# Kernel tuning notes

Hardware: AMD Instinct MI355X
Metric: run time of the kernel (lower is better)

The kernel has to match this reference:

```python
import jax, jax.numpy as jnp
import numpy as np

N_HEADS = 16
HEAD_DIM = 64
ROPE_BASE = 10000.0


def _apply_rope(x, offset):
    # x: (B, T, H, hd); rotates consecutive pairs (x[2i], x[2i+1]) as complex numbers,
    # matching torch.view_as_complex on reshape(..., -1, 2).
    B, T, H, hd = x.shape
    inv_freq = 1.0 / (ROPE_BASE ** (jnp.arange(0, hd, 2, dtype=jnp.float32) / hd))  # (hd/2,)
    t = jnp.arange(T, dtype=jnp.float32) + offset
    ang = t[:, None] * inv_freq[None, :]                      # (T, hd/2)
    cos = jnp.cos(ang)[None, :, None, :]                      # (1, T, 1, hd/2)
    sin = jnp.sin(ang)[None, :, None, :]
    x1 = x[..., 0::2]
    x2 = x[..., 1::2]
    out = jnp.stack([x1 * cos - x2 * sin, x1 * sin + x2 * cos], axis=-1)
    return out.reshape(B, T, H, hd).astype(x.dtype)


def setup_inputs() -> dict:
    key = jax.random.key(0)
    ks = jax.random.split(key, 5)
    D = N_HEADS * HEAD_DIM  # 1024
    s = 1.0 / np.sqrt(D)
    x = jax.random.normal(ks[0], (2, 2048, D), jnp.float32)
    Wqkv = jax.random.normal(ks[1], (D, 3 * D), jnp.float32) * s
    bqkv = jax.random.normal(ks[2], (3 * D,), jnp.float32) * 0.01
    Wout = jax.random.normal(ks[3], (D, D), jnp.float32) * s
    bout = jax.random.normal(ks[4], (D,), jnp.float32) * 0.01
    return {"x": x, "Wqkv": Wqkv, "bqkv": bqkv, "Wout": Wout, "bout": bout, "offset": 0}


def reference(x, Wqkv, bqkv, Wout, bout, offset):
    B, T, D = x.shape
    qkv = (x @ Wqkv + bqkv).reshape(B, T, 3, N_HEADS, HEAD_DIM)
    q, k, v = qkv[:, :, 0], qkv[:, :, 1], qkv[:, :, 2]       # (B, T, H, hd)
    q = _apply_rope(q, offset)
    k = _apply_rope(k, offset)
    # kv_cache is None and T == window_size, so no crop occurs.
    new_cache = jnp.stack([k, v], axis=1)                     # (B, 2, T, H, hd)
    scale = 1.0 / np.sqrt(HEAD_DIM)
    scores = jnp.einsum("bqhd,bkhd->bhqk", q, k) * scale      # (B, H, T, T)
    mask = jnp.tril(jnp.ones((T, T), dtype=bool))
    scores = jnp.where(mask[None, None], scores, jnp.finfo(scores.dtype).min)
    attn = jax.nn.softmax(scores, axis=-1)
    ctx = jnp.einsum("bhqk,bkhd->bqhd", attn, v).reshape(B, T, D)
    out = ctx @ Wout + bout
    return (out, new_cache)
```

## Files before the change

### kernel.cpp

```cpp
#include <hip/hip_runtime.h>
#include <stdint.h>
#include <math.h>


typedef __bf16 bf16_t;
typedef bf16_t bf16x8 __attribute__((ext_vector_type(8)));
typedef float f32x4 __attribute__((ext_vector_type(4)));
typedef unsigned short ushort8_t __attribute__((ext_vector_type(8)));

__device__ __forceinline__ unsigned short f2bf(float f) {
    union { float f; unsigned int i; } v; v.f = f;
    unsigned int r = v.i + 0x7fffu + ((v.i >> 16) & 1u);
    return (unsigned short)(r >> 16);
}
__device__ __forceinline__ bf16x8 ld8(const unsigned short* p) {
    return *(const bf16x8*)p;
}
__device__ __forceinline__ void gload_lds16(const unsigned short* g, unsigned short* l) {
    __builtin_amdgcn_global_load_lds(
        (__attribute__((address_space(1))) void*)(g),
        (__attribute__((address_space(3))) void*)(l),
        16, 0, 0);
}

__global__ void k_cvt(const float* __restrict__ in, unsigned short* __restrict__ out) {
    const int i = (blockIdx.x * 256 + threadIdx.x) * 8;
    float4 a = *(const float4*)&in[i];
    float4 b = *(const float4*)&in[i + 4];
    ushort8_t v;
    v[0] = f2bf(a.x); v[1] = f2bf(a.y); v[2] = f2bf(a.z); v[3] = f2bf(a.w);
    v[4] = f2bf(b.x); v[5] = f2bf(b.y); v[6] = f2bf(b.z); v[7] = f2bf(b.w);
    *(ushort8_t*)&out[i] = v;
}

__global__ void k_ropetab(float* __restrict__ tab, const int* __restrict__ offp) {
    int idx = blockIdx.x * blockDim.x + threadIdx.x;
    int t = idx >> 5, i = idx & 31;
    float off = (float)(*offp);
    float inv = powf(10000.0f, -(float)(2 * i) / 64.0f);
    float ang = ((float)t + off) * inv;
    float s, c;
    sincosf(ang, &s, &c);
    tab[idx * 2]     = c;
    tab[idx * 2 + 1] = s;
}

__global__ void k_transposeF2B(const float* __restrict__ in,
                               unsigned short* __restrict__ out, int R, int C) {
    __shared__ __align__(16) float tile[64 * 68];
    const int bz = blockIdx.z;
    const size_t base = (size_t)bz * R * C;
    const int tR = blockIdx.y * 64, tC = blockIdx.x * 64;
    const int tid = threadIdx.x;
#pragma unroll
    for (int it = 0; it < 4; ++it) {
        int flat = (it * 256 + tid) * 4;
        int r = flat >> 6, c = flat & 63;
        *(float4*)&tile[r * 68 + c] =
            *(const float4*)&in[base + (size_t)(tR + r) * C + tC + c];
    }
    __syncthreads();
#pragma unroll
    for (int it = 0; it < 2; ++it) {
        int flat = (it * 256 + tid) * 8;
        int rr = flat >> 6, cc = flat & 63;
        ushort8_t v;
#pragma unroll
        for (int j = 0; j < 8; ++j) v[j] = f2bf(tile[(cc + j) * 68 + rr]);
        *(ushort8_t*)&out[base + (size_t)(tC + rr) * R + tR + cc] = v;
    }
}

__global__ void k_transpose64(const unsigned short* __restrict__ in,
                              unsigned short* __restrict__ out, int R, int C) {
    __shared__ __align__(16) unsigned short tile[64 * 72];
    const int bz = blockIdx.z;
    const size_t base = (size_t)bz * R * C;
    const int tR = blockIdx.y * 64, tC = blockIdx.x * 64;
    const int tid = threadIdx.x;
#pragma unroll
    for (int it = 0; it < 2; ++it) {
        int flat = (it * 256 + tid) * 8;
        int r = flat >> 6, c = flat & 63;
        *(ushort8_t*)&tile[r * 72 + c] =
            *(const ushort8_t*)&in[base + (size_t)(tR + r) * C + tC + c];
    }
    __syncthreads();
#pragma unroll
    for (int it = 0; it < 2; ++it) {
        int flat = (it * 256 + tid) * 8;
        int rr = flat >> 6, cc = flat & 63;
        ushort8_t v;
#pragma unroll
        for (int j = 0; j < 8; ++j) v[j] = tile[(cc + j) * 72 + rr];
        *(ushort8_t*)&out[base + (size_t)(tC + rr) * R + tR + cc] = v;
    }
}

template <int EPI>
__global__ __launch_bounds__(512, 2) void k_gemm(
    const unsigned short* __restrict__ A,
    const unsigned short* __restrict__ Bt,
    const float* __restrict__ bias,
    const float* __restrict__ tab,
    unsigned short* __restrict__ oq,
    unsigned short* __restrict__ ok,
    unsigned short* __restrict__ ov,
    float* __restrict__ cache,
    float* __restrict__ outp)
{
    constexpr int K = 1024;
    __shared__ __align__(16) unsigned short lds[65536];
    unsigned short* lA = lds;
    unsigned short* lB = lds + 32768;

    const int tid  = threadIdx.x;
    const int lane = tid & 63, w = tid >> 6;
    const int wr = w >> 2, wc = w & 3;
    const int lrow = lane & 15, quad = lane >> 4;

    const int gx  = gridDim.x;
    const int nwg = gx * gridDim.y;
    const int bid = blockIdx.y * gx + blockIdx.x;
    const int sw  = (bid & 7) * (nwg >> 3) + (bid >> 3);
    const int blockM = (sw / gx) * 256;
    const int blockN = (sw % gx) * 256;

    const int q8    = (lane & 7) ^ (lane >> 3);
    const int srow0 = ((w * 16 + (lane >> 3)) << 1) + ((q8 >> 2) & 1);
    const int scol  = (q8 & 3) * 8;
    const unsigned short* srcA = A  + (size_t)(blockM + srow0) * K + scol;
    const unsigned short* srcB = Bt + (size_t)(blockN + srow0) * K + scol;
    unsigned short* dA = lA + w * 1024;
    unsigned short* dB = lB + w * 1024;

    const int rp   = lrow >> 1;
    const int swzu = ((((lane & 1) << 6) | (quad << 4)) ^ (rp << 4)) >> 1;

    f32x4 acc[8][4];
#pragma unroll
    for (int m = 0; m < 8; ++m)
#pragma unroll
        for (int n = 0; n < 4; ++n) acc[m][n] = (f32x4){0.f, 0.f, 0.f, 0.f};

#define STAGE_A(T, KH) do { \
        const unsigned short* s_ = srcA + (T) * 64 + (KH) * 32; \
        unsigned short* d_ = dA + (((2*(T)+(KH)) & 3) << 13); \
        gload_lds16(s_, d_); \
        gload_lds16(s_ + 16 * K, d_ + 512); } while (0)
#define STAGE_B(T, KH) do { \
        const unsigned short* s_ = srcB + (T) * 64 + (KH) * 32; \
        unsigned short* d_ = dB + (((2*(T)+(KH)) & 3) << 13); \
        gload_lds16(s_, d_); \
        gload_lds16(s_ + 16 * K, d_ + 512); } while (0)
#define WAITN(n) asm volatile("s_waitcnt vmcnt(" #n ")" ::: "memory")
#define RD_A(slot) do { \
        _Pragma("unroll") \
        for (int m = 0; m < 8; ++m) \
            aA[m] = ld8(&lA[((slot) << 13) + (wr * 64 + m * 8 + rp) * 64 + swzu]); } while (0)
#define RD_B(slot, nh) do { \
        _Pragma("unroll") \
        for (int nl = 0; nl < 2; ++nl) \
            bB[nl] = ld8(&lB[((slot) << 13) + (wc * 32 + (nh) * 16 + nl * 8 + rp) * 64 + swzu]); } while (0)
#define MFMA16(nh) do { \
        __builtin_amdgcn_s_barrier(); \
        asm volatile("s_waitcnt lgkmcnt(0)" ::: "memory"); \
        __builtin_amdgcn_sched_barrier(0); \
        __builtin_amdgcn_s_setprio(1); \
        _Pragma("unroll") \
        for (int m = 0; m < 8; ++m) { \
            acc[m][(nh)*2+0] = __builtin_amdgcn_mfma_f32_16x16x32_bf16(aA[m], bB[0], acc[m][(nh)*2+0], 0, 0, 0); \
            acc[m][(nh)*2+1] = __builtin_amdgcn_mfma_f32_16x16x32_bf16(aA[m], bB[1], acc[m][(nh)*2+1], 0, 0, 0); } \
        __builtin_amdgcn_s_setprio(0); \
        __builtin_amdgcn_s_barrier(); } while (0)

    STAGE_A(0, 0); STAGE_B(0, 0);
    STAGE_A(0, 1); STAGE_B(0, 1);
    STAGE_A(1, 0); STAGE_B(1, 0);
    STAGE_A(1, 1);
    asm volatile("s_waitcnt vmcnt(8)" ::: "memory");
    __builtin_amdgcn_s_barrier();

    bf16x8 aA[8], bB[2];
    for (int i = 0; i < 7; ++i) {
        const int E = 2 * i, O = 2 * i + 1;
        WAITN(6); RD_A(0); RD_B(0, 0); STAGE_B(O, 1);     MFMA16(0);
        RD_B(0, 1);                    STAGE_A(E + 2, 0); MFMA16(1);
        WAITN(6); RD_A(1); RD_B(1, 0); STAGE_B(E + 2, 0); MFMA16(0);
        RD_B(1, 1);                    STAGE_A(E + 2, 1); MFMA16(1);
        WAITN(6); RD_A(2); RD_B(2, 0); STAGE_B(E + 2, 1); MFMA16(0);
        RD_B(2, 1);                    STAGE_A(O + 2, 0); MFMA16(1);
        WAITN(6); RD_A(3); RD_B(3, 0); STAGE_B(O + 2, 0); MFMA16(0);
        RD_B(3, 1);                    STAGE_A(O + 2, 1); MFMA16(1);
    }
    WAITN(6); RD_A(0); RD_B(0, 0); STAGE_B(15, 1); MFMA16(0);
    RD_B(0, 1);                                    MFMA16(1);
    WAITN(2); RD_A(1); RD_B(1, 0);                 MFMA16(0);
    RD_B(1, 1);                                    MFMA16(1);
    WAITN(0); RD_A(2); RD_B(2, 0);                 MFMA16(0);
    RD_B(2, 1);                                    MFMA16(1);
    RD_A(3); RD_B(3, 0);                           MFMA16(0);
    RD_B(3, 1);                                    MFMA16(1);
#undef STAGE_A
#undef STAGE_B
#undef WAITN
#undef RD_A
#undef RD_B
#undef MFMA16

#pragma unroll
    for (int m = 0; m < 8; ++m) {
        const int rbase = blockM + wr * 128 + m * 16 + quad * 4;
#pragma unroll
        for (int n = 0; n < 4; ++n) {
            const int gcol = blockN + wc * 64 + n * 16 + lrow;
            const float bv = bias[gcol];
#pragma unroll
            for (int r = 0; r < 4; ++r) {
                const int row = rbase + r;
                float val = acc[m][n][r] + bv;
                if (EPI == 0) {
                    outp[(size_t)row * 1024 + gcol] = val;
                } else {
                    const int s = gcol >> 10;
                    const int cn = gcol & 1023;
                    const int h = cn >> 6, d = cn & 63;
                    const int b = row >> 11, t = row & 2047;
                    if (s < 2) {
                        const int ii = d >> 1;
                        const float cz = tab[t * 64 + 2 * ii];
                        const float sz = tab[t * 64 + 2 * ii + 1];
                        const float pv = __shfl_xor(val, 1);
                        val = (d & 1) ? (pv * sz + val * cz) : (val * cz - pv * sz);
                    }
                    const unsigned short r16 = f2bf(val);
                    const size_t bhtd = (((size_t)(b * 16 + h)) * 2048 + t) * 64 + d;
                    if (s == 0) {
                        oq[bhtd] = r16;
                    } else if (s == 1) {
                        ok[bhtd] = r16;
                        cache[(((size_t)(b * 2 + 0)) * 2048 + t) * 1024 + h * 64 + d] = val;
                    } else {
                        ov[bhtd] = r16;
                        cache[(((size_t)(b * 2 + 1)) * 2048 + t) * 1024 + h * 64 + d] = val;
                    }
                }
            }
        }
    }
}

__global__ __launch_bounds__(512, 2) void k_attn(
    const unsigned short* __restrict__ qh,
    const unsigned short* __restrict__ kh,
    const unsigned short* __restrict__ vt,
    unsigned short* __restrict__ ctx)
{
    __shared__ __align__(16) unsigned short lK[2][64 * 64];
    __shared__ __align__(16) unsigned short lV[2][64 * 64];
    __shared__ __align__(16) unsigned short lP[8][32 * 68];
    const int tid = threadIdx.x;
    const int wave = tid >> 6, lane = tid & 63;
    const int lrow = lane & 15, quad = lane >> 4;
    const int sub = lane >> 3, g8 = lane & 7;
    const int grp = g8 ^ (sub & 7);
    const int pj = blockIdx.x;
    const int h = blockIdx.y, b = blockIdx.z;
    const unsigned short* Q  = qh + (size_t)(b * 16 + h) * 2048 * 64;
    const unsigned short* Kp = kh + (size_t)(b * 16 + h) * 2048 * 64;
    const unsigned short* Vt = vt + (size_t)(b * 16 + h) * 64 * 2048;

    const int grpq = wave >> 2;
    const int wv   = wave & 3;
    const int qb   = grpq ? pj : (15 - pj);
    const int qw   = qb * 128 + wv * 32;
    const int nT   = 2 * (16 - pj);

    bf16x8 bOnes;
#pragma unroll
    for (int j = 0; j < 8; ++j) bOnes[j] = (bf16_t)1.0f;

    bf16x8 aQ[2][2];
#pragma unroll
    for (int mf = 0; mf < 2; ++mf)
#pragma unroll
        for (int ks = 0; ks < 2; ++ks) {
            bf16x8 t = ld8(&Q[(size_t)(qw + mf * 16 + lrow) * 64 + ks * 32 + quad * 8]);
#pragma unroll
            for (int j = 0; j < 8; ++j) t[j] = (bf16_t)((float)t[j] * 0.125f);
            aQ[mf][ks] = t;
        }

    f32x4 o[2][4];
#pragma unroll
    for (int mf = 0; mf < 2; ++mf)
#pragma unroll
        for (int i = 0; i < 4; ++i) o[mf][i] = (f32x4){0.f, 0.f, 0.f, 0.f};
    f32x4 lacc[2];
    lacc[0] = (f32x4){0.f, 0.f, 0.f, 0.f};
    lacc[1] = (f32x4){0.f, 0.f, 0.f, 0.f};

    {
        const int c = wave;
        gload_lds16(&Kp[(size_t)(c * 8 + sub) * 64 + grp * 8], &lK[0][c * 512]);
        gload_lds16(&Vt[(size_t)(c * 8 + sub) * 2048 + grp * 8], &lV[0][c * 512]);
    }

    int buf = 0;
    for (int it = 0; it < nT; ++it) {
        const int kt0 = it * 64;
        __syncthreads();
        if (it + 1 < nT) {
            const int kn = kt0 + 64;
            const int c = wave;
            gload_lds16(&Kp[(size_t)(kn + c * 8 + sub) * 64 + grp * 8], &lK[buf ^ 1][c * 512]);
            gload_lds16(&Vt[(size_t)(c * 8 + sub) * 2048 + kn + grp * 8], &lV[buf ^ 1][c * 512]);
        }
        if (kt0 < qw + 32) {
            const unsigned short* lKb = lK[buf];
            const unsigned short* lVb = lV[buf];
            f32x4 s[2][4];
#pragma unroll
            for (int mf = 0; mf < 2; ++mf)
#pragma unroll
                for (int i = 0; i < 4; ++i) s[mf][i] = (f32x4){0.f, 0.f, 0.f, 0.f};
#pragma unroll
            for (int nt = 0; nt < 4; ++nt) {
                const int row = nt * 16 + lrow;
#pragma unroll
                for (int ks = 0; ks < 2; ++ks) {
                    bf16x8 bK = ld8(&lKb[row * 64 + (((ks * 4 + quad) ^ (row & 7)) * 8)]);
#pragma unroll
                    for (int mf = 0; mf < 2; ++mf)
                        s[mf][nt] = __builtin_amdgcn_mfma_f32_16x16x32_bf16(
                            aQ[mf][ks], bK, s[mf][nt], 0, 0, 0);
                }
            }
            if (kt0 + 63 > qw) {
#pragma unroll
                for (int mf = 0; mf < 2; ++mf)
#pragma unroll
                    for (int nt = 0; nt < 4; ++nt) {
                        const int colg = kt0 + nt * 16 + lrow;
#pragma unroll
                        for (int r = 0; r < 4; ++r) {
                            const int rowg = qw + mf * 16 + quad * 4 + r;
                            const float pv = (colg <= rowg) ? __expf(s[mf][nt][r]) : 0.f;
                            lP[wave][(mf * 16 + quad * 4 + r) * 68 + nt * 16 + lrow] = f2bf(pv);
                        }
                    }
            } else {
#pragma unroll
                for (int mf = 0; mf < 2; ++mf)
#pragma unroll
                    for (int nt = 0; nt < 4; ++nt)
#pragma unroll
                        for (int r = 0; r < 4; ++r)
                            lP[wave][(mf * 16 + quad * 4 + r) * 68 + nt * 16 + lrow] =
                                f2bf(__expf(s[mf][nt][r]));
            }
            bf16x8 aP[2][2];
#pragma unroll
            for (int mf = 0; mf < 2; ++mf)
#pragma unroll
                for (int ks = 0; ks < 2; ++ks)
                    aP[mf][ks] = ld8(&lP[wave][(mf * 16 + lrow) * 68 + ks * 32 + quad * 8]);
#pragma unroll
            for (int mf = 0; mf < 2; ++mf)
#pragma unroll
                for (int ks = 0; ks < 2; ++ks)
                    lacc[mf] = __builtin_amdgcn_mfma_f32_16x16x32_bf16(
                        aP[mf][ks], bOnes, lacc[mf], 0, 0, 0);
#pragma unroll
            for (int dt = 0; dt < 4; ++dt) {
                const int row = dt * 16 + lrow;
#pragma unroll
                for (int ks = 0; ks < 2; ++ks) {
                    bf16x8 bV = ld8(&lVb[row * 64 + (((ks * 4 + quad) ^ (row & 7)) * 8)]);
#pragma unroll
                    for (int mf = 0; mf < 2; ++mf)
                        o[mf][dt] = __builtin_amdgcn_mfma_f32_16x16x32_bf16(
                            aP[mf][ks], bV, o[mf][dt], 0, 0, 0);
                }
            }
        }
        buf ^= 1;
    }

    float inv[2][4];
#pragma unroll
    for (int mf = 0; mf < 2; ++mf)
#pragma unroll
        for (int r = 0; r < 4; ++r) inv[mf][r] = 1.0f / lacc[mf][r];
#pragma unroll
    for (int mf = 0; mf < 2; ++mf)
#pragma unroll
        for (int dt = 0; dt < 4; ++dt) {
            const int col = h * 64 + dt * 16 + lrow;
#pragma unroll
            for (int r = 0; r < 4; ++r) {
                const int trow = qw + mf * 16 + quad * 4 + r;
                ctx[((size_t)(b * 2048 + trow)) * 1024 + col] = f2bf(o[mf][dt][r] * inv[mf][r]);
            }
        }
}

extern "C" void kernel_launch(void* const* d_in, const int* in_sizes, int n_in,
                              void* d_out, int out_size, void* d_ws, size_t ws_size,
                              hipStream_t stream) {
    (void)in_sizes; (void)n_in; (void)out_size; (void)ws_size;
    const float* x    = (const float*)d_in[0];
    const float* wqkv = (const float*)d_in[1];
    const float* bqkv = (const float*)d_in[2];
    const float* wout = (const float*)d_in[3];
    const float* bout = (const float*)d_in[4];
    const int*   offp = (const int*)d_in[5];

    float* out   = (float*)d_out;
    float* cache = out + (size_t)2 * 2048 * 1024;

    char* w = (char*)d_ws;
    float* tab            = (float*)w;          w += (size_t)2048 * 64 * sizeof(float);
    unsigned short* xb    = (unsigned short*)w; w += (size_t)4194304 * 2;
    unsigned short* wqkvT = (unsigned short*)w; w += (size_t)3072 * 1024 * 2;
    unsigned short* woutT = (unsigned short*)w; w += (size_t)1024 * 1024 * 2;
    unsigned short* qh    = (unsigned short*)w; w += (size_t)4194304 * 2;
    unsigned short* kh    = (unsigned short*)w; w += (size_t)4194304 * 2;
    unsigned short* vh    = (unsigned short*)w; w += (size_t)4194304 * 2;
    unsigned short* vt    = (unsigned short*)w; w += (size_t)4194304 * 2;
    unsigned short* ctx   = (unsigned short*)w; w += (size_t)4194304 * 2;

    k_ropetab<<<dim3(256), dim3(256), 0, stream>>>(tab, offp);
    k_cvt<<<dim3(2048), dim3(256), 0, stream>>>(x, xb);
    k_transposeF2B<<<dim3(48, 16, 1), dim3(256), 0, stream>>>(wqkv, wqkvT, 1024, 3072);
    k_transposeF2B<<<dim3(16, 16, 1), dim3(256), 0, stream>>>(wout, woutT, 1024, 1024);
    k_gemm<1><<<dim3(12, 16), dim3(512), 0, stream>>>(xb, wqkvT, bqkv, tab, qh, kh, vh, cache, nullptr);
    k_transpose64<<<dim3(1, 32, 32), dim3(256), 0, stream>>>(vh, vt, 2048, 64);
    k_attn<<<dim3(8, 16, 2), dim3(512), 0, stream>>>(qh, kh, vt, ctx);
    k_gemm<0><<<dim3(4, 16), dim3(512), 0, stream>>>(ctx, woutT, bout, tab, nullptr, nullptr, nullptr, nullptr, out);
}
```

Before: 256.4 us.

## Deepen attention K/V prefetch to a 4-slot ring and trim GEMM waits

The attention kernel moves from double-buffered K/V tiles to a 4-slot LDS ring with prefetch distance 2. It waits with explicit vmcnt counts and a raw s_barrier instead of __syncthreads, and raises wave priority around the MFMA blocks. The QKV GEMM main loop also drops every other vmcnt wait, so fewer global-load stalls are exposed. The larger K/V buffers raise the attention kernel's LDS use to roughly 99KB per block, which may no longer allow two 512-thread blocks per CU. Removing GEMM waits also risks reading LDS tiles before their loads land.

```diff
diff --git a/kernel.cpp b/kernel.cpp
--- a/kernel.cpp
+++ b/kernel.cpp
@@ -186,16 +186,16 @@
         const int E = 2 * i, O = 2 * i + 1;
         WAITN(6); RD_A(0); RD_B(0, 0); STAGE_B(O, 1);     MFMA16(0);
         RD_B(0, 1);                    STAGE_A(E + 2, 0); MFMA16(1);
-        WAITN(6); RD_A(1); RD_B(1, 0); STAGE_B(E + 2, 0); MFMA16(0);
+        RD_A(1); RD_B(1, 0);           STAGE_B(E + 2, 0); MFMA16(0);
         RD_B(1, 1);                    STAGE_A(E + 2, 1); MFMA16(1);
         WAITN(6); RD_A(2); RD_B(2, 0); STAGE_B(E + 2, 1); MFMA16(0);
         RD_B(2, 1);                    STAGE_A(O + 2, 0); MFMA16(1);
-        WAITN(6); RD_A(3); RD_B(3, 0); STAGE_B(O + 2, 0); MFMA16(0);
+        RD_A(3); RD_B(3, 0);           STAGE_B(O + 2, 0); MFMA16(0);
         RD_B(3, 1);                    STAGE_A(O + 2, 1); MFMA16(1);
     }
     WAITN(6); RD_A(0); RD_B(0, 0); STAGE_B(15, 1); MFMA16(0);
     RD_B(0, 1);                                    MFMA16(1);
-    WAITN(2); RD_A(1); RD_B(1, 0);                 MFMA16(0);
+    RD_A(1); RD_B(1, 0);                           MFMA16(0);
     RD_B(1, 1);                                    MFMA16(1);
     WAITN(0); RD_A(2); RD_B(2, 0);                 MFMA16(0);
     RD_B(2, 1);                                    MFMA16(1);
@@ -256,8 +256,8 @@
     const unsigned short* __restrict__ vt,
     unsigned short* __restrict__ ctx)
 {
-    __shared__ __align__(16) unsigned short lK[2][64 * 64];
-    __shared__ __align__(16) unsigned short lV[2][64 * 64];
+    __shared__ __align__(16) unsigned short lK[4][64 * 64];
+    __shared__ __align__(16) unsigned short lV[4][64 * 64];
     __shared__ __align__(16) unsigned short lP[8][32 * 68];
     const int tid = threadIdx.x;
     const int wave = tid >> 6, lane = tid & 63;
@@ -300,30 +300,35 @@
     lacc[0] = (f32x4){0.f, 0.f, 0.f, 0.f};
     lacc[1] = (f32x4){0.f, 0.f, 0.f, 0.f};
 
-    {
-        const int c = wave;
-        gload_lds16(&Kp[(size_t)(c * 8 + sub) * 64 + grp * 8], &lK[0][c * 512]);
-        gload_lds16(&Vt[(size_t)(c * 8 + sub) * 2048 + grp * 8], &lV[0][c * 512]);
-    }
-
-    int buf = 0;
+#define STAGE_T(t) do { \
+        const int c_ = wave, s_ = (t) & 3; \
+        gload_lds16(&Kp[(size_t)((t) * 64 + c_ * 8 + sub) * 64 + grp * 8], &lK[s_][c_ * 512]); \
+        gload_lds16(&Vt[(size_t)(c_ * 8 + sub) * 2048 + (t) * 64 + grp * 8], &lV[s_][c_ * 512]); } while (0)
+
+    STAGE_T(0);
+    STAGE_T(1);
+
     for (int it = 0; it < nT; ++it) {
+        if (it + 2 < nT) {
+            STAGE_T(it + 2);
+            asm volatile("s_waitcnt vmcnt(4)" ::: "memory");
+        } else if (it + 1 < nT) {
+            asm volatile("s_waitcnt vmcnt(2)" ::: "memory");
+        } else {
+            asm volatile("s_waitcnt vmcnt(0)" ::: "memory");
+        }
+        __builtin_amdgcn_s_barrier();
+        __builtin_amdgcn_sched_barrier(0);
         const int kt0 = it * 64;
-        __syncthreads();
-        if (it + 1 < nT) {
-            const int kn = kt0 + 64;
-            const int c = wave;
-            gload_lds16(&Kp[(size_t)(kn + c * 8 + sub) * 64 + grp * 8], &lK[buf ^ 1][c * 512]);
-            gload_lds16(&Vt[(size_t)(c * 8 + sub) * 2048 + kn + grp * 8], &lV[buf ^ 1][c * 512]);
-        }
         if (kt0 < qw + 32) {
-            const unsigned short* lKb = lK[buf];
-            const unsigned short* lVb = lV[buf];
+            const unsigned short* lKb = lK[it & 3];
+            const unsigned short* lVb = lV[it & 3];
             f32x4 s[2][4];
 #pragma unroll
             for (int mf = 0; mf < 2; ++mf)
 #pragma unroll
                 for (int i = 0; i < 4; ++i) s[mf][i] = (f32x4){0.f, 0.f, 0.f, 0.f};
+            __builtin_amdgcn_s_setprio(1);
 #pragma unroll
             for (int nt = 0; nt < 4; ++nt) {
                 const int row = nt * 16 + lrow;
@@ -336,6 +341,7 @@
                             aQ[mf][ks], bK, s[mf][nt], 0, 0, 0);
                 }
             }
+            __builtin_amdgcn_s_setprio(0);
             if (kt0 + 63 > qw) {
 #pragma unroll
                 for (int mf = 0; mf < 2; ++mf)
@@ -365,6 +371,7 @@
 #pragma unroll
                 for (int ks = 0; ks < 2; ++ks)
                     aP[mf][ks] = ld8(&lP[wave][(mf * 16 + lrow) * 68 + ks * 32 + quad * 8]);
+            __builtin_amdgcn_s_setprio(1);
 #pragma unroll
             for (int mf = 0; mf < 2; ++mf)
 #pragma unroll
@@ -383,9 +390,10 @@
                             aP[mf][ks], bV, o[mf][dt], 0, 0, 0);
                 }
             }
+            __builtin_amdgcn_s_setprio(0);
         }
-        buf ^= 1;
-    }
+    }
+#undef STAGE_T
 
     float inv[2][4];
 #pragma unroll
```

After: 250.2 us. 2.4% less time.
